# Kernel optimization log

Hardware: AMD Instinct MI355X
Metric: run time of the kernel (lower is better)

The kernel has to match this reference:

```python
import jax, jax.numpy as jnp
import numpy as np
from jax import lax

# Production-scale dims: batch, seq_len, tag_size (incl. START/STOP tags)
B, S, T = 512, 512, 64


def setup_inputs() -> dict:
    key = jax.random.key(0)
    k1, k2, k3, k4 = jax.random.split(key, 4)
    feats = jax.random.normal(k1, (B, S, T), dtype=jnp.float32)
    # prefix-contiguous mask (module assumes mask[:, 0] == 1 and length-style masks)
    lengths = jax.random.randint(k2, (B,), S // 2, S + 1)
    mask = jnp.arange(S)[None, :] < lengths[:, None]  # (B, S) bool
    tags = jax.random.randint(k3, (B, S), 0, T - 2)  # gold tags exclude START/STOP
    transitions = jax.random.normal(k4, (T, T), dtype=jnp.float32) * 0.1
    return {"feats": feats, "mask": mask, "tags": tags, "transitions": transitions}


def _crf_nll(feats, transitions, mask, tags):
    b, s, t = feats.shape
    START, STOP = t - 2, t - 1  # START_TAG = -2, STOP_TAG = -1

    # ---- forward (log partition), matches _calculate_PZ ----
    # partition init: scores[0][:, START, :] = feats[:,0,:] + transitions[START, :]
    init = feats[:, 0, :] + transitions[START][None, :]  # (b, t)

    feats_t = jnp.swapaxes(feats, 0, 1)  # (s, b, t)
    mask_t = jnp.swapaxes(mask, 0, 1)    # (s, b)

    def step(partition, inp):
        f_t, m_t = inp  # (b, t), (b,)
        # cur_values[b, from, to] = feats_t[b, to] + transitions[from, to] + partition[b, from]
        cur = partition[:, :, None] + transitions[None, :, :] + f_t[:, None, :]
        new_p = jax.nn.logsumexp(cur, axis=1)  # reduce over 'from' -> (b, t)
        partition = jnp.where(m_t[:, None], new_p, partition)
        return partition, None

    partition, _ = lax.scan(step, init, (feats_t[1:], mask_t[1:]))

    # final transition to STOP
    final = jax.nn.logsumexp(partition[:, :, None] + transitions[None, :, :], axis=1)
    forward_score = final[:, STOP].sum()

    # ---- gold score, matches _score_sentence ----
    prev = jnp.concatenate(
        [jnp.full((b, 1), START, dtype=tags.dtype), tags[:, :-1]], axis=1
    )  # (b, s): previous tag, START at position 0
    emit = jnp.take_along_axis(feats, tags[:, :, None], axis=2)[:, :, 0]  # (b, s)
    tg_energy = emit + transitions[prev, tags]  # (b, s)
    gold = jnp.where(mask, tg_energy, jnp.zeros((), feats.dtype)).sum()
    lengths = mask.sum(axis=1).astype(jnp.int32)  # (b,)
    end_ids = jnp.take_along_axis(tags, (lengths - 1)[:, None].astype(tags.dtype), axis=1)[:, 0]
    gold = gold + transitions[end_ids, STOP].sum()

    # average_batch = False
    return forward_score - gold


def reference(feats, mask, tags, transitions):
    return _crf_nll(feats, transitions, mask, tags)
```

## Files before the change

### kernel.cpp

```cpp
#include <hip/hip_runtime.h>

#define BB 512
#define SS 512
#define TT 64
#define START_TAG 62
#define STOP_TAG 63

#define LOG2E 1.4426950408889634f
#define LN2   0.6931471805599453f

__device__ __forceinline__ float bcast0(float x) {
    return __int_as_float(__builtin_amdgcn_readfirstlane(__float_as_int(x)));
}
__device__ __forceinline__ float rlane(float x, int l) {
    return __int_as_float(__builtin_amdgcn_readlane(__float_as_int(x), l));
}

__device__ __forceinline__ float matvec64(const float E, const float (&vt)[64]) {
    float a0 = 0.f, a1 = 0.f, a2 = 0.f, a3 = 0.f;
    float t[2][8];
    #pragma unroll
    for (int j = 0; j < 8; ++j) t[0][j] = rlane(E, j);
    #pragma unroll
    for (int g = 0; g < 8; ++g) {
        const int cur = g & 1, nxt = cur ^ 1;
        if (g < 7) {
            #pragma unroll
            for (int j = 0; j < 8; ++j) t[nxt][j] = rlane(E, 8 * g + 8 + j);
        }
        a0 = fmaf(t[cur][0], vt[8 * g + 0], a0);
        a1 = fmaf(t[cur][1], vt[8 * g + 1], a1);
        a2 = fmaf(t[cur][2], vt[8 * g + 2], a2);
        a3 = fmaf(t[cur][3], vt[8 * g + 3], a3);
        a0 = fmaf(t[cur][4], vt[8 * g + 4], a0);
        a1 = fmaf(t[cur][5], vt[8 * g + 5], a1);
        a2 = fmaf(t[cur][6], vt[8 * g + 6], a2);
        a3 = fmaf(t[cur][7], vt[8 * g + 7], a3);
    }
    return (a0 + a1) + (a2 + a3);
}

__global__ void __launch_bounds__(128)
__attribute__((amdgpu_waves_per_eu(1, 1))) crf_main(
    const float* __restrict__ feats, const int* __restrict__ mask,
    const int* __restrict__ tags, const float* __restrict__ trans,
    float* __restrict__ out)
{
    const int b    = blockIdx.x;
    const int tid  = threadIdx.x;
    const int lane = tid & 63;

    const float* frow = feats + (size_t)b * SS * TT;
    const int*   mrow = mask + b * SS;

    if (tid < 64) {
        int cnt = 0;
        #pragma unroll
        for (int s = lane; s < SS; s += 64) cnt += (mrow[s] != 0);
        #pragma unroll
        for (int off = 32; off; off >>= 1) cnt += __shfl_xor(cnt, off);
        const int len = cnt;

        float vt[64];
        #pragma unroll
        for (int i = 0; i < 64; ++i)
            vt[i] = __builtin_amdgcn_exp2f(trans[i * TT + lane] * LOG2E);

        const float P0   = frow[lane] + trans[START_TAG * TT + lane];
        const float offs = bcast0(P0);
        float E = __builtin_amdgcn_exp2f((P0 - offs) * LOG2E);
        int ksum = 0;

        float fr[8];
        #pragma unroll
        for (int j = 0; j < 8; ++j) {
            int r = 1 + j; if (r > SS - 1) r = SS - 1;
            fr[j] = frow[(size_t)r * TT + lane];
        }

        int s = 1;
        for (; s + 3 < len; s += 4) {
            float n0, n1, n2, n3;
            {
                int r0 = s + 8, r1 = s + 9, r2 = s + 10, r3 = s + 11;
                if (r0 > SS - 1) r0 = SS - 1;
                if (r1 > SS - 1) r1 = SS - 1;
                if (r2 > SS - 1) r2 = SS - 1;
                if (r3 > SS - 1) r3 = SS - 1;
                n0 = frow[(size_t)r0 * TT + lane];
                n1 = frow[(size_t)r1 * TT + lane];
                n2 = frow[(size_t)r2 * TT + lane];
                n3 = frow[(size_t)r3 * TT + lane];
            }

            #pragma unroll
            for (int j = 0; j < 3; ++j) {
                const float fe = __builtin_amdgcn_exp2f(fr[j] * LOG2E);
                const float D  = matvec64(E, vt);
                E = fe * D;
            }
            {
                const float fe = __builtin_amdgcn_exp2f(fr[3] * LOG2E);
                const float D  = matvec64(E, vt);
                const int ebits = (__builtin_amdgcn_readfirstlane(
                                       __float_as_int(D)) >> 23) & 0xff;
                ksum += ebits - 127;
                const float scale = __int_as_float((254 - ebits) << 23);
                E = fe * (D * scale);
            }

            #pragma unroll
            for (int j = 0; j < 4; ++j) fr[j] = fr[j + 4];
            fr[4] = n0; fr[5] = n1; fr[6] = n2; fr[7] = n3;
        }

        const int rem = len - s;
        #pragma unroll
        for (int j = 0; j < 3; ++j) {
            if (j < rem) {
                const float fe = __builtin_amdgcn_exp2f(fr[j] * LOG2E);
                const float D  = matvec64(E, vt);
                const int ebits = (__builtin_amdgcn_readfirstlane(
                                       __float_as_int(D)) >> 23) & 0xff;
                ksum += ebits - 127;
                const float scale = __int_as_float((254 - ebits) << 23);
                E = fe * (D * scale);
            }
        }

        const float ts = __builtin_amdgcn_exp2f(trans[lane * TT + STOP_TAG] * LOG2E);
        float e = E * ts;
        #pragma unroll
        for (int off = 32; off; off >>= 1) e += __shfl_xor(e, off);

        if (lane == 0)
            atomicAdd(out, offs + (float)ksum * LN2
                           + LN2 * __builtin_amdgcn_logf(e));
    } else {
        const int* trow = tags + b * SS;
        int   cnt = 0;
        float acc = 0.f;
        for (int s = lane; s < SS; s += 64) {
            if (mrow[s] != 0) {
                ++cnt;
                const int tag  = trow[s];
                const int prev = (s == 0) ? START_TAG : trow[s - 1];
                acc += frow[(size_t)s * TT + tag] + trans[prev * TT + tag];
            }
        }
        #pragma unroll
        for (int off = 32; off; off >>= 1) {
            acc += __shfl_xor(acc, off);
            cnt += __shfl_xor(cnt, off);
        }
        if (lane == 0) {
            const int end_id = trow[cnt - 1];
            atomicAdd(out, -(acc + trans[end_id * TT + STOP_TAG]));
        }
    }
}

__global__ void zero_out(float* out) { out[0] = 0.f; }

extern "C" void kernel_launch(void* const* d_in, const int* in_sizes, int n_in,
                              void* d_out, int out_size, void* d_ws, size_t ws_size,
                              hipStream_t stream) {
    const float* feats = (const float*)d_in[0];
    const int*   mask  = (const int*)d_in[1];
    const int*   tags  = (const int*)d_in[2];
    const float* trans = (const float*)d_in[3];
    float* out = (float*)d_out;

    zero_out<<<1, 1, 0, stream>>>(out);
    crf_main<<<BB, 128, 0, stream>>>(feats, mask, tags, trans, out);
}
```

Baseline: 205.6 us.

## Use fp16 dot2 matvec with LDS-broadcast state instead of readlane fp32 FMAs

Replaces the 64 readlane broadcasts plus 64 fp32 FMAs per step with the state vector held in fp16 in shared memory, read as vectorized h8 loads, and multiplied by the exp-transition matrix packed into fp16 pairs using v_dot2 instructions. Renormalization now happens every step instead of every fourth step, so fp16 does not overflow. This halves the multiply count and removes the scalar readlane bottleneck on the serial recurrence. In exchange it adds an LDS write/read round-trip per step and loses precision from storing the state and transition exponentials in fp16. There is no barrier between the LDS write and the next read, so it relies on single-wave ordering.

```diff
diff --git a/kernel.cpp b/kernel.cpp
--- a/kernel.cpp
+++ b/kernel.cpp
@@ -9,35 +9,46 @@
 #define LOG2E 1.4426950408889634f
 #define LN2   0.6931471805599453f
 
+typedef _Float16 h2 __attribute__((ext_vector_type(2)));
+typedef _Float16 h8 __attribute__((ext_vector_type(8)));
+
 __device__ __forceinline__ float bcast0(float x) {
     return __int_as_float(__builtin_amdgcn_readfirstlane(__float_as_int(x)));
 }
-__device__ __forceinline__ float rlane(float x, int l) {
-    return __int_as_float(__builtin_amdgcn_readlane(__float_as_int(x), l));
+
+__device__ __forceinline__ float matvec_dot(const _Float16* Ebuf,
+                                            const h2 (&Mh)[32]) {
+    float a0 = 0.f, a1 = 0.f, a2 = 0.f, a3 = 0.f;
+    float a4 = 0.f, a5 = 0.f, a6 = 0.f, a7 = 0.f;
+    h8 v[8];
+    #pragma unroll
+    for (int j = 0; j < 8; ++j) v[j] = *(const h8*)(Ebuf + 8 * j);
+    #pragma unroll
+    for (int j = 0; j < 8; ++j) {
+        const h2 p0 = __builtin_shufflevector(v[j], v[j], 0, 1);
+        const h2 p1 = __builtin_shufflevector(v[j], v[j], 2, 3);
+        const h2 p2 = __builtin_shufflevector(v[j], v[j], 4, 5);
+        const h2 p3 = __builtin_shufflevector(v[j], v[j], 6, 7);
+        a0 = __builtin_amdgcn_fdot2(p0, Mh[4 * j + 0], a0, false);
+        a1 = __builtin_amdgcn_fdot2(p1, Mh[4 * j + 1], a1, false);
+        a2 = __builtin_amdgcn_fdot2(p2, Mh[4 * j + 2], a2, false);
+        a3 = __builtin_amdgcn_fdot2(p3, Mh[4 * j + 3], a3, false);
+        const float t = a0; a0 = a4; a4 = t;
+        const float u = a1; a1 = a5; a5 = u;
+        const float w = a2; a2 = a6; a6 = w;
+        const float x = a3; a3 = a7; a7 = x;
+    }
+    return ((a0 + a1) + (a2 + a3)) + ((a4 + a5) + (a6 + a7));
 }
 
-__device__ __forceinline__ float matvec64(const float E, const float (&vt)[64]) {
-    float a0 = 0.f, a1 = 0.f, a2 = 0.f, a3 = 0.f;
-    float t[2][8];
-    #pragma unroll
-    for (int j = 0; j < 8; ++j) t[0][j] = rlane(E, j);
-    #pragma unroll
-    for (int g = 0; g < 8; ++g) {
-        const int cur = g & 1, nxt = cur ^ 1;
-        if (g < 7) {
-            #pragma unroll
-            for (int j = 0; j < 8; ++j) t[nxt][j] = rlane(E, 8 * g + 8 + j);
-        }
-        a0 = fmaf(t[cur][0], vt[8 * g + 0], a0);
-        a1 = fmaf(t[cur][1], vt[8 * g + 1], a1);
-        a2 = fmaf(t[cur][2], vt[8 * g + 2], a2);
-        a3 = fmaf(t[cur][3], vt[8 * g + 3], a3);
-        a0 = fmaf(t[cur][4], vt[8 * g + 4], a0);
-        a1 = fmaf(t[cur][5], vt[8 * g + 5], a1);
-        a2 = fmaf(t[cur][6], vt[8 * g + 6], a2);
-        a3 = fmaf(t[cur][7], vt[8 * g + 7], a3);
-    }
-    return (a0 + a1) + (a2 + a3);
+#define STEP(FRJ) { \
+    const float fe = __builtin_amdgcn_exp2f((FRJ) * LOG2E); \
+    const float D  = matvec_dot(Ebuf, Mh); \
+    const int eb = (__builtin_amdgcn_readfirstlane(__float_as_int(D)) \
+                    >> 23) & 0xff; \
+    ksum += eb - 127; \
+    const float scale = __int_as_float((254 - eb) << 23); \
+    Ebuf[lane] = (_Float16)(fe * (D * scale)); \
 }
 
 __global__ void __launch_bounds__(128)
@@ -53,6 +64,8 @@
     const float* frow = feats + (size_t)b * SS * TT;
     const int*   mrow = mask + b * SS;
 
+    __shared__ __align__(16) _Float16 Ebuf[TT];
+
     if (tid < 64) {
         int cnt = 0;
         #pragma unroll
@@ -61,14 +74,20 @@
         for (int off = 32; off; off >>= 1) cnt += __shfl_xor(cnt, off);
         const int len = cnt;
 
-        float vt[64];
+        h2 Mh[32];
         #pragma unroll
-        for (int i = 0; i < 64; ++i)
-            vt[i] = __builtin_amdgcn_exp2f(trans[i * TT + lane] * LOG2E);
+        for (int p = 0; p < 32; ++p) {
+            const float m0 =
+                __builtin_amdgcn_exp2f(trans[(2 * p) * TT + lane] * LOG2E);
+            const float m1 =
+                __builtin_amdgcn_exp2f(trans[(2 * p + 1) * TT + lane] * LOG2E);
+            Mh[p][0] = (_Float16)m0;
+            Mh[p][1] = (_Float16)m1;
+        }
 
         const float P0   = frow[lane] + trans[START_TAG * TT + lane];
         const float offs = bcast0(P0);
-        float E = __builtin_amdgcn_exp2f((P0 - offs) * LOG2E);
+        Ebuf[lane] = (_Float16)__builtin_amdgcn_exp2f((P0 - offs) * LOG2E);
         int ksum = 0;
 
         float fr[8];
@@ -93,21 +112,7 @@
                 n3 = frow[(size_t)r3 * TT + lane];
             }
 
-            #pragma unroll
-            for (int j = 0; j < 3; ++j) {
-                const float fe = __builtin_amdgcn_exp2f(fr[j] * LOG2E);
-                const float D  = matvec64(E, vt);
-                E = fe * D;
-            }
-            {
-                const float fe = __builtin_amdgcn_exp2f(fr[3] * LOG2E);
-                const float D  = matvec64(E, vt);
-                const int ebits = (__builtin_amdgcn_readfirstlane(
-                                       __float_as_int(D)) >> 23) & 0xff;
-                ksum += ebits - 127;
-                const float scale = __int_as_float((254 - ebits) << 23);
-                E = fe * (D * scale);
-            }
+            STEP(fr[0]) STEP(fr[1]) STEP(fr[2]) STEP(fr[3])
 
             #pragma unroll
             for (int j = 0; j < 4; ++j) fr[j] = fr[j + 4];
@@ -115,21 +120,14 @@
         }
 
         const int rem = len - s;
-        #pragma unroll
-        for (int j = 0; j < 3; ++j) {
-            if (j < rem) {
-                const float fe = __builtin_amdgcn_exp2f(fr[j] * LOG2E);
-                const float D  = matvec64(E, vt);
-                const int ebits = (__builtin_amdgcn_readfirstlane(
-                                       __float_as_int(D)) >> 23) & 0xff;
-                ksum += ebits - 127;
-                const float scale = __int_as_float((254 - ebits) << 23);
-                E = fe * (D * scale);
-            }
-        }
+        if (rem > 0) { STEP(fr[0]) }
+        if (rem > 1) { STEP(fr[1]) }
+        if (rem > 2) { STEP(fr[2]) }
 
-        const float ts = __builtin_amdgcn_exp2f(trans[lane * TT + STOP_TAG] * LOG2E);
-        float e = E * ts;
+        const float Ev = (float)Ebuf[lane];
+        const float Ms =
+            __builtin_amdgcn_exp2f(trans[lane * TT + STOP_TAG] * LOG2E);
+        float e = Ev * Ms;
         #pragma unroll
         for (int off = 32; off; off >>= 1) e += __shfl_xor(e, off);
 
```

Result: faster. 174.8 us (-15.0%).
